# Optimization experiments

Hardware: AMD Instinct MI355X
Metric: run time of the kernel (lower is better)

## Reference

```python
import jax, jax.numpy as jnp
import numpy as np

LOG_EPS = 1e-30
MIN_EPS = 1e-8
N_CLASS = 19
GAMMA = 1.0        # focal_gamma
ADAPT_B = 0.2
ADAPT_A = 0.9      # beta (a_decay == 0)
ADAPT_D = 8.0
CONF_THRESH = 0.8  # uda_confidence_thresh


def setup_inputs() -> dict:
    key = jax.random.key(0)
    k1, k2 = jax.random.split(key)
    N, C, H, W = 2, N_CLASS, 512, 1024
    logits_before = jax.random.normal(k1, (N, C, H, W), jnp.float32)
    logits_after = jax.random.normal(k2, (N, C, H, W), jnp.float32)
    cls_thresh = jnp.ones((N_CLASS,), jnp.float32) * CONF_THRESH
    return {"logits_before": logits_before, "logits_after": logits_after,
            "cls_thresh": cls_thresh}


def ias_thresh(conf, label, cls_thresh):
    # conf, label: [N,H,W] max-prob and argmax class per pixel
    conf_f = conf.reshape(-1)    # [T]
    label_f = label.reshape(-1)  # [T]

    def per_class(c, thr):
        # class-c confidences, others pushed to the end of the descending sort
        vals = jnp.where(label_f == c, conf_f, -jnp.inf)
        ext = jnp.concatenate([vals, thr[None]])  # append current threshold
        srt = -jnp.sort(-ext)                     # descending
        count = jnp.sum(label_f == c)
        # index = int(len_extend * adapt_b * thresh**adapt_d); len_extend = count+1
        idx = jnp.floor((count + 1).astype(jnp.float32) * ADAPT_B * thr ** ADAPT_D).astype(jnp.int32)
        return srt[idx]  # count==0 -> idx==0 -> picks thr (matches torch branch)

    return jax.vmap(per_class)(jnp.arange(N_CLASS), cls_thresh)


def reference(logits_before, logits_after, cls_thresh):
    pb = jax.nn.softmax(logits_before, axis=1)
    pa = jax.nn.softmax(logits_after, axis=1)
    pb_d = jax.lax.stop_gradient(pb)
    log_pb_d = jnp.log(pb_d + LOG_EPS)
    log_pa = jnp.log(pa + LOG_EPS)

    bma = 1.0 - pa  # focal_type == 1: ones_like(pb_d) - pa
    label = jnp.argmax(pb_d, axis=1)  # [N,H,W]
    conf = jnp.max(pb_d, axis=1)      # [N,H,W]
    # scatter(select_mask)+sum == gather the argmax channel
    sel_diff = jnp.take_along_axis(bma, label[:, None], axis=1)  # [N,1,H,W]

    loss_kldiv = pb_d * (log_pb_d - jnp.abs(sel_diff) ** GAMMA * log_pa)
    loss_entropy = -pb * jnp.log(pb + LOG_EPS)
    loss = jnp.sum(loss_kldiv + loss_entropy, axis=1)  # [N,H,W]

    tmp = ias_thresh(conf, label, cls_thresh)
    new_thresh = ADAPT_A * cls_thresh + (1.0 - ADAPT_A) * tmp
    new_thresh = jnp.where(new_thresh >= 1.0, 0.999, new_thresh)

    pix_thresh = new_thresh[label]           # [N,H,W]
    mask = conf > pix_thresh
    adapt_ratio = jnp.mean(mask.astype(jnp.float32))
    solid_ratio = jnp.mean((conf > CONF_THRESH).astype(jnp.float32))

    # loss[mask] -> clamp -> mean, expressed as a masked mean (jit-safe)
    num = jnp.sum(jnp.where(mask, jnp.maximum(loss, MIN_EPS), 0.0))
    den = jnp.maximum(jnp.sum(mask).astype(loss.dtype), 1.0)
    return num / den, adapt_ratio, solid_ratio
```

## Files before the change

kernel.cpp:

```cpp
#include <hip/hip_runtime.h>
#include <math.h>

#define NCLS 19
#define HW   (512*1024)
#define CHW  (NCLS*HW)
#define TPIX (2*HW)
#define NB   512
#define NPART 16
#define CAND_MAX 4096

#define WS_PART   0
#define WS_CANDC  622592
#define WS_ACCUM  622720
#define WS_ZSTART 622592
#define WS_ZSIZE  256
#define WS_SEL    622848
#define WS_NEWTH  623360
#define WS_CONF   623616
#define WS_LOSS   4817920
#define WS_LABEL  9012224
#define WS_CAND   10060800

#define WAVE_PX 64
#define WPB 4
__global__ __launch_bounds__(256)
void k1_pixel(const float* __restrict__ lb_t, const float* __restrict__ la_t,
              float* __restrict__ conf_o, float* __restrict__ loss_o,
              unsigned char* __restrict__ label_o)
{
    __shared__ float smem[WPB * 2 * NCLS * WAVE_PX];
    const int tid  = threadIdx.x;
    const int wave = tid >> 6;
    const int lane = tid & 63;
    const int tile = blockIdx.x * WPB + wave;
    const int pix  = tile * WAVE_PX + lane;
    const int n    = pix >> 19;
    const int rem  = pix & (HW - 1);
    const float* lb = lb_t + (size_t)n * CHW + rem;
    const float* la = la_t + (size_t)n * CHW + rem;
    float* sw = &smem[wave * (2 * NCLS * WAVE_PX)];

#pragma unroll
    for (int c = 0; c < NCLS; ++c) {
        __builtin_amdgcn_global_load_lds(
            (__attribute__((address_space(1))) void*)(lb + (size_t)c * HW),
            (__attribute__((address_space(3))) void*)(sw + c * WAVE_PX),
            4, 0, 0);
    }
#pragma unroll
    for (int c = 0; c < NCLS; ++c) {
        __builtin_amdgcn_global_load_lds(
            (__attribute__((address_space(1))) void*)(la + (size_t)c * HW),
            (__attribute__((address_space(3))) void*)(sw + (NCLS + c) * WAVE_PX),
            4, 0, 0);
    }
    asm volatile("s_waitcnt vmcnt(0)" ::: "memory");

    float mb, zb, dot, a_lab, ma, za; int lab;
    {
        float bb = sw[lane];
        float aa = sw[NCLS * WAVE_PX + lane];
        mb = bb; zb = 1.0f; dot = aa; lab = 0; a_lab = aa; ma = aa; za = 1.0f;
    }
#pragma unroll
    for (int c = 1; c < NCLS; ++c) {
        float b = sw[c * WAVE_PX + lane];
        float a = sw[(NCLS + c) * WAVE_PX + lane];
        float mn = fmaxf(mb, b);
        float eo = __expf(mb - mn);
        float en = __expf(b - mn);
        zb  = zb * eo + en;
        dot = dot * eo + en * a;
        bool upd = b > mb;
        lab   = upd ? c : lab;
        a_lab = upd ? a : a_lab;
        mb = mn;
        float mna = fmaxf(ma, a);
        za = za * __expf(ma - mna) + __expf(a - mna);
        ma = mna;
    }

    float cf = 1.0f / zb;
    float pa_lab = __expf(a_lab - ma) / za;
    float ls = (1.0f - pa_lab) * (ma + __logf(za) - dot / zb);

    conf_o[pix]  = cf;
    loss_o[pix]  = ls;
    label_o[pix] = (unsigned char)lab;
}

__global__ __launch_bounds__(256)
void k1b_hist(const float4* __restrict__ conf, const uchar4* __restrict__ label,
              unsigned int* __restrict__ part)
{
    __shared__ unsigned int lh[NCLS * NB];
    const int t = threadIdx.x;
    for (int w = t; w < NCLS * NB; w += 256) lh[w] = 0u;
    __syncthreads();

    const int per_blk4 = TPIX / 4 / NPART;
    const int base4 = blockIdx.x * per_blk4;
    for (int i = 0; i < per_blk4 / 256; ++i) {
        int g = base4 + i * 256 + t;
        float4 c4 = conf[g];
        uchar4 l4 = label[g];
        float cf[4] = {c4.x, c4.y, c4.z, c4.w};
        int   lb[4] = {l4.x, l4.y, l4.z, l4.w};
#pragma unroll
        for (int k = 0; k < 4; ++k) {
            int bin = (int)(cf[k] * (float)NB);
            bin = bin < (NB - 1) ? bin : (NB - 1);
            atomicAdd(&lh[lb[k] * NB + bin], 1u);
        }
    }
    __syncthreads();

    unsigned int* dst = part + blockIdx.x * (NCLS * NB);
    for (int w = t; w < NCLS * NB; w += 256) dst[w] = lh[w];
}

__global__ __launch_bounds__(256)
void k2_select(const unsigned int* __restrict__ part, const float* __restrict__ cls_thresh,
               int* __restrict__ sel, unsigned int* __restrict__ cand_cnt,
               float* __restrict__ cand)
{
    int c = blockIdx.x;
    int t = threadIdx.x;
    float thr = cls_thresh[c];
    int thr_bin = (int)(thr * (float)NB); thr_bin = thr_bin < (NB-1) ? thr_bin : (NB-1);

    int base = NB - (t + 1) * 2;
    unsigned h0 = 0, h1 = 0;
    for (int b = 0; b < NPART; ++b) {
        const unsigned int* p = part + b * (NCLS * NB) + c * NB;
        h0 += p[base];
        h1 += p[base + 1];
    }
    if (base == thr_bin)     h0 += 1u;
    if (base + 1 == thr_bin) h1 += 1u;
    unsigned s = h0 + h1;

    __shared__ unsigned sc[256];
    sc[t] = s;
    __syncthreads();
    for (int off = 1; off < 256; off <<= 1) {
        unsigned vt = sc[t];
        unsigned vp = (t >= off) ? sc[t - off] : 0u;
        __syncthreads();
        sc[t] = vt + vp;
        __syncthreads();
    }
    unsigned total_ext = sc[255];
    unsigned cnt = total_ext - 1u;
    int idx = (int)floorf((float)(cnt + 1u) * 0.2f * powf(thr, 8.0f));

    unsigned above = sc[t] - s;
    if ((unsigned)idx >= above && (unsigned)idx < above + s) {
        int B, r;
        if ((unsigned)idx < above + h1) { B = base + 1; r = (int)((unsigned)idx - above); }
        else                            { B = base;     r = (int)((unsigned)idx - above - h1); }
        sel[2 * c]     = B;
        sel[2 * c + 1] = r;
        if (B == thr_bin) {
            unsigned pos = atomicAdd(&cand_cnt[c], 1u);
            if (pos < CAND_MAX) cand[c * CAND_MAX + pos] = thr;
        }
    }
}

__global__ __launch_bounds__(256)
void k3_gather(const float4* __restrict__ conf, const uchar4* __restrict__ label,
               const int* __restrict__ sel, unsigned int* __restrict__ cand_cnt,
               float* __restrict__ cand)
{
    int g = blockIdx.x * 256 + threadIdx.x;
    float4 c4 = conf[g];
    uchar4 l4 = label[g];
    float cf[4] = {c4.x, c4.y, c4.z, c4.w};
    int   lb[4] = {l4.x, l4.y, l4.z, l4.w};
#pragma unroll
    for (int i = 0; i < 4; ++i) {
        int bin = (int)(cf[i] * (float)NB);
        bin = bin < (NB - 1) ? bin : (NB - 1);
        if (bin == sel[2 * lb[i]]) {
            unsigned pos = atomicAdd(&cand_cnt[lb[i]], 1u);
            if (pos < CAND_MAX) cand[lb[i] * CAND_MAX + pos] = cf[i];
        }
    }
}

__global__ __launch_bounds__(256)
void k4_thresh(const int* __restrict__ sel, const unsigned int* __restrict__ cand_cnt,
               const float* __restrict__ cand, const float* __restrict__ cls_thresh,
               float* __restrict__ newth)
{
    int c = blockIdx.x;
    int t = threadIdx.x;
    unsigned mc = cand_cnt[c];
    int m = (int)(mc < (unsigned)CAND_MAX ? mc : (unsigned)CAND_MAX);
    int r = sel[2 * c + 1];

    __shared__ float v[CAND_MAX];
    __shared__ float result;
    for (int i = t; i < m; i += 256) v[i] = cand[c * CAND_MAX + i];
    __syncthreads();

    for (int i = t; i < m; i += 256) {
        float x = v[i];
        int gcnt = 0, e = 0;
        for (int j = 0; j < m; ++j) {
            gcnt += (v[j] > x);
            e    += (v[j] == x);
        }
        if (gcnt <= r && r < gcnt + e) result = x;
    }
    __syncthreads();
    if (t == 0) {
        float thr = cls_thresh[c];
        float nt = 0.9f * thr + 0.1f * result;
        if (nt >= 1.0f) nt = 0.999f;
        newth[c] = nt;
    }
}

__global__ __launch_bounds__(256)
void k5_reduce(const float4* __restrict__ conf, const float4* __restrict__ loss,
               const uchar4* __restrict__ label, const float* __restrict__ newth,
               float* __restrict__ accum)
{
    __shared__ float th[NCLS];
    if (threadIdx.x < NCLS) th[threadIdx.x] = newth[threadIdx.x];
    __syncthreads();

    int g = blockIdx.x * 256 + threadIdx.x;
    float4 c4 = conf[g];
    float4 s4 = loss[g];
    uchar4 l4 = label[g];
    float cf[4] = {c4.x, c4.y, c4.z, c4.w};
    float lv[4] = {s4.x, s4.y, s4.z, s4.w};
    int   lb[4] = {l4.x, l4.y, l4.z, l4.w};

    float ls = 0.0f; int mask = 0, solid = 0;
#pragma unroll
    for (int i = 0; i < 4; ++i) {
        bool m = cf[i] > th[lb[i]];
        mask  += m ? 1 : 0;
        solid += (cf[i] > 0.8f) ? 1 : 0;
        ls    += m ? fmaxf(lv[i], 1e-8f) : 0.0f;
    }

    for (int off = 32; off > 0; off >>= 1) {
        ls    += __shfl_down(ls, off, 64);
        mask  += __shfl_down(mask, off, 64);
        solid += __shfl_down(solid, off, 64);
    }
    __shared__ float s_ls[4];
    __shared__ int   s_m[4], s_s[4];
    int w = threadIdx.x >> 6;
    if ((threadIdx.x & 63) == 0) { s_ls[w] = ls; s_m[w] = mask; s_s[w] = solid; }
    __syncthreads();
    if (threadIdx.x == 0) {
        float L = s_ls[0] + s_ls[1] + s_ls[2] + s_ls[3];
        int   M = s_m[0] + s_m[1] + s_m[2] + s_m[3];
        int   S = s_s[0] + s_s[1] + s_s[2] + s_s[3];
        atomicAdd(&accum[0], L);
        atomicAdd(&((unsigned int*)accum)[1], (unsigned)M);
        atomicAdd(&((unsigned int*)accum)[2], (unsigned)S);
    }
}

__global__ void k6_out(const float* __restrict__ accum, float* __restrict__ out)
{
    float sum = accum[0];
    unsigned cm = ((const unsigned int*)accum)[1];
    unsigned cs = ((const unsigned int*)accum)[2];
    float den = fmaxf((float)cm, 1.0f);
    out[0] = sum / den;
    out[1] = (float)cm / (float)TPIX;
    out[2] = (float)cs / (float)TPIX;
}

extern "C" void kernel_launch(void* const* d_in, const int* in_sizes, int n_in,
                              void* d_out, int out_size, void* d_ws, size_t ws_size,
                              hipStream_t stream)
{
    const float* lb  = (const float*)d_in[0];
    const float* la  = (const float*)d_in[1];
    const float* cth = (const float*)d_in[2];
    float* out = (float*)d_out;

    char* ws = (char*)d_ws;
    unsigned int* part     = (unsigned int*)(ws + WS_PART);
    unsigned int* cand_cnt = (unsigned int*)(ws + WS_CANDC);
    float*        accum    = (float*)(ws + WS_ACCUM);
    int*          sel      = (int*)(ws + WS_SEL);
    float*        newth    = (float*)(ws + WS_NEWTH);
    float*        conf     = (float*)(ws + WS_CONF);
    float*        loss     = (float*)(ws + WS_LOSS);
    unsigned char* label   = (unsigned char*)(ws + WS_LABEL);
    float*        cand     = (float*)(ws + WS_CAND);

    hipMemsetAsync(ws + WS_ZSTART, 0, WS_ZSIZE, stream);

    dim3 blk(256);
    dim3 grd1(TPIX / (WPB * WAVE_PX));
    dim3 grd4(TPIX / 4 / 256);

    k1_pixel<<<grd1, blk, 0, stream>>>(lb, la, conf, loss, label);
    k1b_hist<<<NPART, blk, 0, stream>>>((const float4*)conf, (const uchar4*)label, part);
    k2_select<<<NCLS, blk, 0, stream>>>(part, cth, sel, cand_cnt, cand);
    k3_gather<<<grd4, blk, 0, stream>>>((const float4*)conf, (const uchar4*)label,
                                        sel, cand_cnt, cand);
    k4_thresh<<<NCLS, blk, 0, stream>>>(sel, cand_cnt, cand, cth, newth);
    k5_reduce<<<grd4, blk, 0, stream>>>((const float4*)conf, (const float4*)loss,
                                        (const uchar4*)label, newth, accum);
    k6_out<<<1, 1, 0, stream>>>(accum, out);
}
```

Baseline: 260.4 us.

## Fuse select/thresh/out stages via last-block pattern and use 16-byte LDS loads

Merges the histogram with class selection, the candidate gather with the threshold search, and the final reduction with output writing. Each merge uses a last-block-done atomic counter, which removes the memset and three kernel launches. The pixel kernel now loads 16-byte chunks per lane into a block-wide 256-pixel LDS tile, and partial histograms are stored as ushort with twice as many partitions. The threshold search switches from an O(m^2) rank over all candidates to a sub-histogram that narrows the search to a small bucket. In exchange, the last-block tails run serially on one block, and zeroing the counters inside block 0 of k1 relies on stream ordering.

```diff
diff --git a/kernel.cpp b/kernel.cpp
--- a/kernel.cpp
+++ b/kernel.cpp
@@ -6,14 +6,15 @@
 #define CHW  (NCLS*HW)
 #define TPIX (2*HW)
 #define NB   512
-#define NPART 16
+#define NPART 32
 #define CAND_MAX 4096
+#define SUBB 1024
+#define SCAP 256
 
 #define WS_PART   0
 #define WS_CANDC  622592
 #define WS_ACCUM  622720
-#define WS_ZSTART 622592
-#define WS_ZSIZE  256
+#define WS_DONE   622784
 #define WS_SEL    622848
 #define WS_NEWTH  623360
 #define WS_CONF   623616
@@ -21,51 +22,55 @@
 #define WS_LABEL  9012224
 #define WS_CAND   10060800
 
-#define WAVE_PX 64
-#define WPB 4
+#define TILE 256
 __global__ __launch_bounds__(256)
 void k1_pixel(const float* __restrict__ lb_t, const float* __restrict__ la_t,
               float* __restrict__ conf_o, float* __restrict__ loss_o,
-              unsigned char* __restrict__ label_o)
+              unsigned char* __restrict__ label_o,
+              unsigned int* __restrict__ cand_cnt,
+              unsigned int* __restrict__ accum_u,
+              unsigned int* __restrict__ done)
 {
-    __shared__ float smem[WPB * 2 * NCLS * WAVE_PX];
-    const int tid  = threadIdx.x;
-    const int wave = tid >> 6;
-    const int lane = tid & 63;
-    const int tile = blockIdx.x * WPB + wave;
-    const int pix  = tile * WAVE_PX + lane;
-    const int n    = pix >> 19;
-    const int rem  = pix & (HW - 1);
+    __shared__ float smem[2 * NCLS * TILE];
+    const int tid = threadIdx.x;
+    if (blockIdx.x == 0) {
+        if (tid < NCLS)            cand_cnt[tid] = 0u;
+        else if (tid < NCLS + 3)   accum_u[tid - NCLS] = 0u;
+        else if (tid < NCLS + 6)   done[tid - NCLS - 3] = 0u;
+    }
+    const int wave = tid >> 6, lane = tid & 63;
+    const int tb  = blockIdx.x * TILE;
+    const int n   = tb >> 19;
+    const int rem = tb & (HW - 1);
     const float* lb = lb_t + (size_t)n * CHW + rem;
     const float* la = la_t + (size_t)n * CHW + rem;
-    float* sw = &smem[wave * (2 * NCLS * WAVE_PX)];
 
 #pragma unroll
-    for (int c = 0; c < NCLS; ++c) {
-        __builtin_amdgcn_global_load_lds(
-            (__attribute__((address_space(1))) void*)(lb + (size_t)c * HW),
-            (__attribute__((address_space(3))) void*)(sw + c * WAVE_PX),
-            4, 0, 0);
-    }
-#pragma unroll
-    for (int c = 0; c < NCLS; ++c) {
-        __builtin_amdgcn_global_load_lds(
-            (__attribute__((address_space(1))) void*)(la + (size_t)c * HW),
-            (__attribute__((address_space(3))) void*)(sw + (NCLS + c) * WAVE_PX),
-            4, 0, 0);
+    for (int i = 0; i < 10; ++i) {
+        int r = wave + 4 * i;
+        if (r < 2 * NCLS) {
+            const float* src = (r < NCLS) ? (lb + (size_t)r * HW)
+                                          : (la + (size_t)(r - NCLS) * HW);
+            __builtin_amdgcn_global_load_lds(
+                (__attribute__((address_space(1))) void*)(src + (lane << 2)),
+                (__attribute__((address_space(3))) void*)(smem + r * TILE),
+                16, 0, 0);
+        }
     }
     asm volatile("s_waitcnt vmcnt(0)" ::: "memory");
-
+    __syncthreads();
+
+    const int pix = tb + tid;
     float mb, zb, dot, a_lab, ma, za; int lab;
     {
-        float bb = sw[lane];
-        float aa = sw[NCLS * WAVE_PX + lane];
+        float bb = smem[tid];
+        float aa = smem[NCLS * TILE + tid];
         mb = bb; zb = 1.0f; dot = aa; lab = 0; a_lab = aa; ma = aa; za = 1.0f;
     }
 #pragma unroll
     for (int c = 1; c < NCLS; ++c) {
-        float b = sw[c * WAVE_PX + lane];
-        float a = sw[(NCLS + c) * WAVE_PX + lane];
+        float b = smem[c * TILE + tid];
+        float a = smem[(NCLS + c) * TILE + tid];
         float mn = fmaxf(mb, b);
         float eo = __expf(mb - mn);
         float en = __expf(b - mn);
@@ -90,17 +95,20 @@
 }
 
 __global__ __launch_bounds__(256)
-void k1b_hist(const float4* __restrict__ conf, const uchar4* __restrict__ label,
-              unsigned int* __restrict__ part)
+void k2_hist_select(const float4* __restrict__ conf, const uchar4* __restrict__ label,
+                    unsigned short* __restrict__ part, const float* __restrict__ cls_thresh,
+                    int* __restrict__ sel, unsigned int* __restrict__ cand_cnt,
+                    float* __restrict__ cand, unsigned int* __restrict__ done)
 {
     __shared__ unsigned int lh[NCLS * NB];
+    __shared__ int s_last;
     const int t = threadIdx.x;
     for (int w = t; w < NCLS * NB; w += 256) lh[w] = 0u;
     __syncthreads();
 
-    const int per_blk4 = TPIX / 4 / NPART;
-    const int base4 = blockIdx.x * per_blk4;
-    for (int i = 0; i < per_blk4 / 256; ++i) {
+    const int per4  = TPIX / 4 / NPART;
+    const int base4 = blockIdx.x * per4;
+    for (int i = 0; i < per4 / 256; ++i) {
         int g = base4 + i * 256 + t;
         float4 c4 = conf[g];
         uchar4 l4 = label[g];
@@ -115,118 +123,195 @@
     }
     __syncthreads();
 
-    unsigned int* dst = part + blockIdx.x * (NCLS * NB);
-    for (int w = t; w < NCLS * NB; w += 256) dst[w] = lh[w];
+    unsigned short* dst = part + blockIdx.x * (NCLS * NB);
+    for (int w = t; w < NCLS * NB; w += 256) dst[w] = (unsigned short)lh[w];
+
+    __threadfence();
+    if (t == 0) s_last = (atomicAdd(&done[0], 1u) == (unsigned)(NPART - 1)) ? 1 : 0;
+    __syncthreads();
+    if (!s_last) return;
+    __threadfence();
+
+    for (int w = t; w < NCLS * NB; w += 256) {
+        unsigned s = 0;
+        for (int b = 0; b < NPART; ++b) s += part[b * (NCLS * NB) + w];
+        lh[w] = s;
+    }
+    __syncthreads();
+
+    const int wave = t >> 6, lane = t & 63;
+    for (int c = wave; c < NCLS; c += 4) {
+        float thr = cls_thresh[c];
+        int thr_bin = (int)(thr * (float)NB); thr_bin = thr_bin < (NB - 1) ? thr_bin : (NB - 1);
+        int cb = NB - 8 * (lane + 1);
+        unsigned hsum = 0;
+        for (int i = 0; i < 8; ++i) {
+            unsigned h = lh[c * NB + cb + i];
+            if (cb + i == thr_bin) h += 1u;
+            hsum += h;
+        }
+        unsigned incl = hsum;
+        for (int off = 1; off < 64; off <<= 1) {
+            unsigned v = __shfl_up(incl, off, 64);
+            if (lane >= off) incl += v;
+        }
+        unsigned total_ext = __shfl(incl, 63, 64);
+        unsigned cnt = total_ext - 1u;
+        int idx = (int)floorf((float)(cnt + 1u) * 0.2f * powf(thr, 8.0f));
+        unsigned above = incl - hsum;
+        if ((unsigned)idx >= above && (unsigned)idx < above + hsum) {
+            unsigned cum = above; int B = thr_bin, r = 0;
+            for (int i = 7; i >= 0; --i) {
+                int bi = cb + i;
+                unsigned h = lh[c * NB + bi];
+                if (bi == thr_bin) h += 1u;
+                if ((unsigned)idx < cum + h) { B = bi; r = (int)((unsigned)idx - cum); break; }
+                cum += h;
+            }
+            sel[2 * c]     = B;
+            sel[2 * c + 1] = r;
+            if (B == thr_bin) {
+                unsigned pos = atomicAdd(&cand_cnt[c], 1u);
+                if (pos < CAND_MAX) cand[c * CAND_MAX + pos] = thr;
+            }
+        }
+    }
 }
 
 __global__ __launch_bounds__(256)
-void k2_select(const unsigned int* __restrict__ part, const float* __restrict__ cls_thresh,
-               int* __restrict__ sel, unsigned int* __restrict__ cand_cnt,
-               float* __restrict__ cand)
+void k3_gather_thresh(const float4* __restrict__ conf, const uchar4* __restrict__ label,
+                      const int* __restrict__ sel, unsigned int* __restrict__ cand_cnt,
+                      float* __restrict__ cand, const float* __restrict__ cls_thresh,
+                      float* __restrict__ newth, unsigned int* __restrict__ done)
 {
-    int c = blockIdx.x;
-    int t = threadIdx.x;
-    float thr = cls_thresh[c];
-    int thr_bin = (int)(thr * (float)NB); thr_bin = thr_bin < (NB-1) ? thr_bin : (NB-1);
-
-    int base = NB - (t + 1) * 2;
-    unsigned h0 = 0, h1 = 0;
-    for (int b = 0; b < NPART; ++b) {
-        const unsigned int* p = part + b * (NCLS * NB) + c * NB;
-        h0 += p[base];
-        h1 += p[base + 1];
-    }
-    if (base == thr_bin)     h0 += 1u;
-    if (base + 1 == thr_bin) h1 += 1u;
-    unsigned s = h0 + h1;
-
-    __shared__ unsigned sc[256];
-    sc[t] = s;
-    __syncthreads();
-    for (int off = 1; off < 256; off <<= 1) {
-        unsigned vt = sc[t];
-        unsigned vp = (t >= off) ? sc[t - off] : 0u;
-        __syncthreads();
-        sc[t] = vt + vp;
-        __syncthreads();
-    }
-    unsigned total_ext = sc[255];
-    unsigned cnt = total_ext - 1u;
-    int idx = (int)floorf((float)(cnt + 1u) * 0.2f * powf(thr, 8.0f));
-
-    unsigned above = sc[t] - s;
-    if ((unsigned)idx >= above && (unsigned)idx < above + s) {
-        int B, r;
-        if ((unsigned)idx < above + h1) { B = base + 1; r = (int)((unsigned)idx - above); }
-        else                            { B = base;     r = (int)((unsigned)idx - above - h1); }
-        sel[2 * c]     = B;
-        sel[2 * c + 1] = r;
-        if (B == thr_bin) {
-            unsigned pos = atomicAdd(&cand_cnt[c], 1u);
-            if (pos < CAND_MAX) cand[c * CAND_MAX + pos] = thr;
+    const int t = threadIdx.x;
+    {
+        int g = blockIdx.x * 256 + t;
+        float4 c4 = conf[g];
+        uchar4 l4 = label[g];
+        float cf[4] = {c4.x, c4.y, c4.z, c4.w};
+        int   lb[4] = {l4.x, l4.y, l4.z, l4.w};
+#pragma unroll
+        for (int i = 0; i < 4; ++i) {
+            int bin = (int)(cf[i] * (float)NB);
+            bin = bin < (NB - 1) ? bin : (NB - 1);
+            if (bin == sel[2 * lb[i]]) {
+                unsigned pos = atomicAdd(&cand_cnt[lb[i]], 1u);
+                if (pos < CAND_MAX) cand[lb[i] * CAND_MAX + pos] = cf[i];
+            }
+        }
+    }
+    __threadfence();
+    __shared__ int s_last;
+    if (t == 0) s_last = (atomicAdd(&done[1], 1u) == (unsigned)(gridDim.x - 1)) ? 1 : 0;
+    __syncthreads();
+    if (!s_last) return;
+    __threadfence();
+
+    __shared__ unsigned int subh[4][SUBB];
+    __shared__ float        sbuf[4][SCAP];
+    __shared__ unsigned int scnt[4];
+    const int wave = t >> 6, lane = t & 63;
+    for (int c = wave; c < NCLS; c += 4) {
+        unsigned mc = cand_cnt[c];
+        int m = (int)(mc < (unsigned)CAND_MAX ? mc : (unsigned)CAND_MAX);
+        int B = sel[2 * c];
+        int r = sel[2 * c + 1];
+        const float* v = cand + c * CAND_MAX;
+
+        for (int i = lane; i < SUBB; i += 64) subh[wave][i] = 0u;
+        if (lane == 0) scnt[wave] = 0u;
+        asm volatile("s_waitcnt lgkmcnt(0)" ::: "memory");
+
+        const float scale = (float)NB;
+        for (int i = lane; i < m; i += 64) {
+            float x = v[i];
+            int s = (int)((x * scale - (float)B) * (float)SUBB);
+            s = s < 0 ? 0 : (s > SUBB - 1 ? SUBB - 1 : s);
+            atomicAdd(&subh[wave][s], 1u);
+        }
+        asm volatile("s_waitcnt lgkmcnt(0)" ::: "memory");
+
+        int cb = SUBB - 16 * (lane + 1);
+        unsigned hsum = 0;
+        for (int i = 0; i < 16; ++i) hsum += subh[wave][cb + i];
+        unsigned incl = hsum;
+        for (int off = 1; off < 64; off <<= 1) {
+            unsigned q = __shfl_up(incl, off, 64);
+            if (lane >= off) incl += q;
+        }
+        unsigned above = incl - hsum;
+        int S = -1; unsigned r2 = 0;
+        if ((unsigned)r >= above && (unsigned)r < above + hsum) {
+            unsigned cum = above;
+            for (int i = 15; i >= 0; --i) {
+                unsigned h = subh[wave][cb + i];
+                if ((unsigned)r < cum + h) { S = cb + i; r2 = (unsigned)r - cum; break; }
+                cum += h;
+            }
+        }
+        unsigned long long bal = __ballot(S >= 0);
+        int wl = (int)__ffsll((unsigned long long)bal) - 1;
+        S  = __shfl(S, wl, 64);
+        r2 = (unsigned)__shfl((int)r2, wl, 64);
+
+        for (int i = lane; i < m; i += 64) {
+            float x = v[i];
+            int s = (int)((x * scale - (float)B) * (float)SUBB);
+            s = s < 0 ? 0 : (s > SUBB - 1 ? SUBB - 1 : s);
+            if (s == S) {
+                unsigned p = atomicAdd(&scnt[wave], 1u);
+                if (p < (unsigned)SCAP) sbuf[wave][p] = x;
+            }
+        }
+        asm volatile("s_waitcnt lgkmcnt(0)" ::: "memory");
+        unsigned cntS = scnt[wave];
+
+        float res = 0.0f; bool have = false;
+        if (cntS <= (unsigned)SCAP) {
+            for (int i = lane; i < (int)cntS; i += 64) {
+                float x = sbuf[wave][i];
+                int gc = 0, e = 0;
+                for (int j = 0; j < (int)cntS; ++j) {
+                    float y = sbuf[wave][j];
+                    gc += (y > x); e += (y == x);
+                }
+                if (gc <= (int)r2 && (int)r2 < gc + e) { res = x; have = true; }
+            }
+        } else {
+            for (int i = lane; i < m; i += 64) {
+                float x = v[i];
+                int s = (int)((x * scale - (float)B) * (float)SUBB);
+                s = s < 0 ? 0 : (s > SUBB - 1 ? SUBB - 1 : s);
+                if (s != S) continue;
+                int gc = 0, e = 0;
+                for (int j = 0; j < m; ++j) {
+                    float y = v[j];
+                    int sj = (int)((y * scale - (float)B) * (float)SUBB);
+                    sj = sj < 0 ? 0 : (sj > SUBB - 1 ? SUBB - 1 : sj);
+                    if (sj != S) continue;
+                    gc += (y > x); e += (y == x);
+                }
+                if (gc <= (int)r2 && (int)r2 < gc + e) { res = x; have = true; }
+            }
+        }
+        unsigned long long hb = __ballot(have);
+        int hl = (int)__ffsll((unsigned long long)hb) - 1;
+        res = __shfl(res, hl, 64);
+        if (lane == 0) {
+            float thr = cls_thresh[c];
+            float nt = 0.9f * thr + 0.1f * res;
+            if (nt >= 1.0f) nt = 0.999f;
+            newth[c] = nt;
         }
     }
 }
 
 __global__ __launch_bounds__(256)
-void k3_gather(const float4* __restrict__ conf, const uchar4* __restrict__ label,
-               const int* __restrict__ sel, unsigned int* __restrict__ cand_cnt,
-               float* __restrict__ cand)
-{
-    int g = blockIdx.x * 256 + threadIdx.x;
-    float4 c4 = conf[g];
-    uchar4 l4 = label[g];
-    float cf[4] = {c4.x, c4.y, c4.z, c4.w};
-    int   lb[4] = {l4.x, l4.y, l4.z, l4.w};
-#pragma unroll
-    for (int i = 0; i < 4; ++i) {
-        int bin = (int)(cf[i] * (float)NB);
-        bin = bin < (NB - 1) ? bin : (NB - 1);
-        if (bin == sel[2 * lb[i]]) {
-            unsigned pos = atomicAdd(&cand_cnt[lb[i]], 1u);
-            if (pos < CAND_MAX) cand[lb[i] * CAND_MAX + pos] = cf[i];
-        }
-    }
-}
-
-__global__ __launch_bounds__(256)
-void k4_thresh(const int* __restrict__ sel, const unsigned int* __restrict__ cand_cnt,
-               const float* __restrict__ cand, const float* __restrict__ cls_thresh,
-               float* __restrict__ newth)
-{
-    int c = blockIdx.x;
-    int t = threadIdx.x;
-    unsigned mc = cand_cnt[c];
-    int m = (int)(mc < (unsigned)CAND_MAX ? mc : (unsigned)CAND_MAX);
-    int r = sel[2 * c + 1];
-
-    __shared__ float v[CAND_MAX];
-    __shared__ float result;
-    for (int i = t; i < m; i += 256) v[i] = cand[c * CAND_MAX + i];
-    __syncthreads();
-
-    for (int i = t; i < m; i += 256) {
-        float x = v[i];
-        int gcnt = 0, e = 0;
-        for (int j = 0; j < m; ++j) {
-            gcnt += (v[j] > x);
-            e    += (v[j] == x);
-        }
-        if (gcnt <= r && r < gcnt + e) result = x;
-    }
-    __syncthreads();
-    if (t == 0) {
-        float thr = cls_thresh[c];
-        float nt = 0.9f * thr + 0.1f * result;
-        if (nt >= 1.0f) nt = 0.999f;
-        newth[c] = nt;
-    }
-}
-
-__global__ __launch_bounds__(256)
-void k5_reduce(const float4* __restrict__ conf, const float4* __restrict__ loss,
-               const uchar4* __restrict__ label, const float* __restrict__ newth,
-               float* __restrict__ accum)
+void k4_reduce_out(const float4* __restrict__ conf, const float4* __restrict__ loss,
+                   const uchar4* __restrict__ label, const float* __restrict__ newth,
+                   float* __restrict__ accum, unsigned int* __restrict__ done,
+                   float* __restrict__ out)
 {
     __shared__ float th[NCLS];
     if (threadIdx.x < NCLS) th[threadIdx.x] = newth[threadIdx.x];
@@ -248,7 +333,6 @@
         solid += (cf[i] > 0.8f) ? 1 : 0;
         ls    += m ? fmaxf(lv[i], 1e-8f) : 0.0f;
     }
-
     for (int off = 32; off > 0; off >>= 1) {
         ls    += __shfl_down(ls, off, 64);
         mask  += __shfl_down(mask, off, 64);
@@ -267,17 +351,20 @@
         atomicAdd(&((unsigned int*)accum)[1], (unsigned)M);
         atomicAdd(&((unsigned int*)accum)[2], (unsigned)S);
     }
-}
-
-__global__ void k6_out(const float* __restrict__ accum, float* __restrict__ out)
-{
-    float sum = accum[0];
-    unsigned cm = ((const unsigned int*)accum)[1];
-    unsigned cs = ((const unsigned int*)accum)[2];
-    float den = fmaxf((float)cm, 1.0f);
-    out[0] = sum / den;
-    out[1] = (float)cm / (float)TPIX;
-    out[2] = (float)cs / (float)TPIX;
+    __threadfence();
+    __shared__ int s_last;
+    if (threadIdx.x == 0) s_last = (atomicAdd(&done[2], 1u) == (unsigned)(gridDim.x - 1)) ? 1 : 0;
+    __syncthreads();
+    if (!s_last) return;
+    __threadfence();
+    if (threadIdx.x == 0) {
+        float sum = accum[0];
+        unsigned cm = ((const unsigned int*)accum)[1];
+        unsigned cs = ((const unsigned int*)accum)[2];
+        out[0] = sum / fmaxf((float)cm, 1.0f);
+        out[1] = (float)cm / (float)TPIX;
+        out[2] = (float)cs / (float)TPIX;
+    }
 }
 
 extern "C" void kernel_launch(void* const* d_in, const int* in_sizes, int n_in,
@@ -290,29 +377,27 @@
     float* out = (float*)d_out;
 
     char* ws = (char*)d_ws;
-    unsigned int* part     = (unsigned int*)(ws + WS_PART);
-    unsigned int* cand_cnt = (unsigned int*)(ws + WS_CANDC);
-    float*        accum    = (float*)(ws + WS_ACCUM);
-    int*          sel      = (int*)(ws + WS_SEL);
-    float*        newth    = (float*)(ws + WS_NEWTH);
-    float*        conf     = (float*)(ws + WS_CONF);
-    float*        loss     = (float*)(ws + WS_LOSS);
-    unsigned char* label   = (unsigned char*)(ws + WS_LABEL);
-    float*        cand     = (float*)(ws + WS_CAND);
-
-    hipMemsetAsync(ws + WS_ZSTART, 0, WS_ZSIZE, stream);
+    unsigned short* part     = (unsigned short*)(ws + WS_PART);
+    unsigned int*   cand_cnt = (unsigned int*)(ws + WS_CANDC);
+    float*          accum    = (float*)(ws + WS_ACCUM);
+    unsigned int*   done     = (unsigned int*)(ws + WS_DONE);
+    int*            sel      = (int*)(ws + WS_SEL);
+    float*          newth    = (float*)(ws + WS_NEWTH);
+    float*          conf     = (float*)(ws + WS_CONF);
+    float*          loss     = (float*)(ws + WS_LOSS);
+    unsigned char*  label    = (unsigned char*)(ws + WS_LABEL);
+    float*          cand     = (float*)(ws + WS_CAND);
 
     dim3 blk(256);
-    dim3 grd1(TPIX / (WPB * WAVE_PX));
+    dim3 grd1(TPIX / TILE);
     dim3 grd4(TPIX / 4 / 256);
 
-    k1_pixel<<<grd1, blk, 0, stream>>>(lb, la, conf, loss, label);
-    k1b_hist<<<NPART, blk, 0, stream>>>((const float4*)conf, (const uchar4*)label, part);
-    k2_select<<<NCLS, blk, 0, stream>>>(part, cth, sel, cand_cnt, cand);
-    k3_gather<<<grd4, blk, 0, stream>>>((const float4*)conf, (const uchar4*)label,
-                                        sel, cand_cnt, cand);
-    k4_thresh<<<NCLS, blk, 0, stream>>>(sel, cand_cnt, cand, cth, newth);
-    k5_reduce<<<grd4, blk, 0, stream>>>((const float4*)conf, (const float4*)loss,
-                                        (const uchar4*)label, newth, accum);
-    k6_out<<<1, 1, 0, stream>>>(accum, out);
+    k1_pixel<<<grd1, blk, 0, stream>>>(lb, la, conf, loss, label,
+                                       cand_cnt, (unsigned int*)accum, done);
+    k2_hist_select<<<NPART, blk, 0, stream>>>((const float4*)conf, (const uchar4*)label,
+                                              part, cth, sel, cand_cnt, cand, done);
+    k3_gather_thresh<<<grd4, blk, 0, stream>>>((const float4*)conf, (const uchar4*)label,
+                                               sel, cand_cnt, cand, cth, newth, done);
+    k4_reduce_out<<<grd4, blk, 0, stream>>>((const float4*)conf, (const float4*)loss,
+                                            (const uchar4*)label, newth, accum, done, out);
 }
```

New measurement: 502.2 us. +92.9%, slower.
